# Optimization experiments

Measured on AMD Instinct MI355X. Metric: run time of the kernel, lower is better.

The kernel has to match this reference:

```python
import jax, jax.numpy as jnp
import numpy as np

N_NODES = 50000
N_REL = 4
N_EDGES = 400000
IN_F, HID_F, OUT_F = 128, 128, 64


def _graphconv(h, s, d, W, b, n_nodes):
    """DGL GraphConv, norm='both': D_dst^{-1/2} A D_src^{-1/2} h W + b.
    Degrees clamped to min 1 (DGL behavior for isolated nodes)."""
    ones = jnp.ones(s.shape[0], h.dtype)
    deg_out = jnp.clip(jax.ops.segment_sum(ones, s, num_segments=n_nodes), 1.0)
    deg_in = jnp.clip(jax.ops.segment_sum(ones, d, num_segments=n_nodes), 1.0)
    # scale src features, transform first (weight applied pre-aggregation)
    hw = (h * jax.lax.rsqrt(deg_out)[:, None]) @ W          # [N, out]
    msg = hw[s]                                              # gather  [E, out]
    agg = jax.ops.segment_sum(msg, d, num_segments=n_nodes)  # scatter [N, out]
    return agg * jax.lax.rsqrt(deg_in)[:, None] + b


def _hetero_layer(h, src, dst, W, b):
    # HeteroGraphConv with aggregate='sum': sum per-relation GraphConv outputs
    n_nodes = h.shape[0]
    out = _graphconv(h, src[0], dst[0], W[0], b[0], n_nodes)
    for r in range(1, W.shape[0]):
        out = out + _graphconv(h, src[r], dst[r], W[r], b[r], n_nodes)
    return out


def setup_inputs() -> dict:
    key = jax.random.key(0)
    k = jax.random.split(key, 6)
    x = jax.random.normal(k[0], (N_NODES, IN_F), dtype=jnp.float32)
    src = jax.random.randint(k[1], (N_REL, N_EDGES), 0, N_NODES, dtype=jnp.int32)
    dst = jax.random.randint(k[2], (N_REL, N_EDGES), 0, N_NODES, dtype=jnp.int32)
    W1 = jax.random.normal(k[3], (N_REL, IN_F, HID_F), dtype=jnp.float32) / np.sqrt(IN_F)
    b1 = jnp.zeros((N_REL, HID_F), dtype=jnp.float32)
    W2 = jax.random.normal(k[4], (N_REL, HID_F, OUT_F), dtype=jnp.float32) / np.sqrt(HID_F)
    b2 = jnp.zeros((N_REL, OUT_F), dtype=jnp.float32)
    return {"x": x, "src": src, "dst": dst, "W1": W1, "b1": b1, "W2": W2, "b2": b2}


def reference(x, src, dst, W1, b1, W2, b2):
    h = _hetero_layer(x, src, dst, W1, b1)
    h = jax.nn.relu(h)
    return _hetero_layer(h, src, dst, W2, b2)
```

## Files before the change

### kernel.cpp

```cpp
#include <hip/hip_runtime.h>
#include <hip/hip_bf16.h>

#define N_NODES 50000
#define N_REL 4
#define N_EDGES 400000
#define CHUNK 1024
#define NCHUNK ((N_NODES + CHUNK - 1) / CHUNK)

#define EB 32
#define ECH (N_EDGES / EB)
#define NR 8
#define RNG (N_NODES / NR)

using short8 = __attribute__((ext_vector_type(8))) short;
using f32x4 = __attribute__((ext_vector_type(4))) float;

static __device__ inline unsigned short f2bf(float f) {
  unsigned u = __float_as_uint(f);
  unsigned r = (u + 0x7FFFu + ((u >> 16) & 1u)) >> 16;
  return (unsigned short)r;
}
static __device__ inline float bf2f(unsigned short b) {
  return __uint_as_float(((unsigned)b) << 16);
}
static __device__ inline void fma_bf2(unsigned w, float ds, float& a0,
                                      float& a1) {
  float lo = __uint_as_float(w << 16);
  float hi = __uint_as_float(w & 0xffff0000u);
  a0 = fmaf(lo, ds, a0);
  a1 = fmaf(hi, ds, a1);
}

__global__ __launch_bounds__(256) void k_hist(const int* __restrict__ src,
                                              const int* __restrict__ dst,
                                              unsigned short* __restrict__ Hs,
                                              unsigned short* __restrict__ Hd) {
  const int range = blockIdx.x % NR;
  const int chunk = (blockIdx.x / NR) % EB;
  const int rel = blockIdx.x / (NR * EB);
  __shared__ unsigned int ldsS[RNG / 2], ldsD[RNG / 2];
  for (int i = threadIdx.x; i < RNG / 2; i += 256) {
    ldsS[i] = 0u;
    ldsD[i] = 0u;
  }
  __syncthreads();
  const int n0 = range * RNG;
  const int* sp = src + (size_t)rel * N_EDGES + chunk * ECH;
  const int* dp = dst + (size_t)rel * N_EDGES + chunk * ECH;
  for (int e = threadIdx.x; e < ECH; e += 256) {
    int s = sp[e] - n0;
    if ((unsigned)s < RNG) atomicAdd(&ldsS[s >> 1], 1u << ((s & 1) * 16));
    int d = dp[e] - n0;
    if ((unsigned)d < RNG) atomicAdd(&ldsD[d >> 1], 1u << ((d & 1) * 16));
  }
  __syncthreads();
  unsigned int* HsO =
      (unsigned int*)(Hs + ((size_t)rel * EB + chunk) * N_NODES + n0);
  unsigned int* HdO =
      (unsigned int*)(Hd + ((size_t)rel * EB + chunk) * N_NODES + n0);
  for (int i = threadIdx.x; i < RNG / 2; i += 256) {
    HsO[i] = ldsS[i];
    HdO[i] = ldsD[i];
  }
}

__global__ __launch_bounds__(256) void k_reduce_m(
    const unsigned short* __restrict__ Hs, unsigned short* __restrict__ Hd,
    int* __restrict__ cnt_m, float* __restrict__ dso,
    float* __restrict__ dsi) {
  int n = blockIdx.x * 256 + threadIdx.x;
  if (n >= N_NODES) return;
#pragma unroll
  for (int r = 0; r < N_REL; ++r) {
    int so = 0;
#pragma unroll
    for (int b = 0; b < EB; ++b) so += Hs[((size_t)r * EB + b) * N_NODES + n];
    dso[r * N_NODES + n] = rsqrtf((float)(so < 1 ? 1 : so));
  }
  int run = 0;
#pragma unroll
  for (int r = 0; r < N_REL; ++r) {
    int start = run;
#pragma unroll
    for (int b = 0; b < EB; ++b) {
      size_t off = ((size_t)r * EB + b) * N_NODES + n;
      int v = Hd[off];
      Hd[off] = (unsigned short)run;
      run += v;
    }
    int di = run - start;
    dsi[r * N_NODES + n] = rsqrtf((float)(di < 1 ? 1 : di));
  }
  cnt_m[n] = run;
}

__global__ __launch_bounds__(256) void k_chunk_sums(
    const int* __restrict__ cnt_m, int* __restrict__ chunkSums) {
  int c = blockIdx.x;
  int t = threadIdx.x;
  int base = c * CHUNK + t * 4;
  int s = 0;
#pragma unroll
  for (int j = 0; j < 4; ++j) {
    int n = base + j;
    if (n < N_NODES) s += cnt_m[n];
  }
  __shared__ int lds[256];
  lds[t] = s;
  __syncthreads();
  for (int off = 128; off > 0; off >>= 1) {
    if (t < off) lds[t] += lds[t + off];
    __syncthreads();
  }
  if (t == 0) chunkSums[c] = lds[0];
}

__global__ __launch_bounds__(64) void k_scan_chunks(int* __restrict__ chunkSums,
                                                    int* __restrict__ row_ptr) {
  if (threadIdx.x == 0) {
    int running = 0;
    for (int c = 0; c < NCHUNK; ++c) {
      int v = chunkSums[c];
      chunkSums[c] = running;
      running += v;
    }
    row_ptr[N_NODES] = N_REL * N_EDGES;
  }
}

__global__ __launch_bounds__(256) void k_scan_within(
    const int* __restrict__ cnt_m, const int* __restrict__ chunkOff,
    int* __restrict__ row_ptr) {
  int c = blockIdx.x;
  int t = threadIdx.x;
  int base = c * CHUNK + t * 4;
  int v[4];
#pragma unroll
  for (int j = 0; j < 4; ++j) {
    int n = base + j;
    v[j] = (n < N_NODES) ? cnt_m[n] : 0;
  }
  int total = v[0] + v[1] + v[2] + v[3];
  __shared__ int lds[256];
  lds[t] = total;
  __syncthreads();
  for (int off = 1; off < 256; off <<= 1) {
    int add = (t >= off) ? lds[t - off] : 0;
    __syncthreads();
    lds[t] += add;
    __syncthreads();
  }
  int thrExcl = lds[t] - total + chunkOff[c];
  int pre = 0;
#pragma unroll
  for (int j = 0; j < 4; ++j) {
    int n = base + j;
    if (n < N_NODES) row_ptr[n] = thrExcl + pre;
    pre += v[j];
  }
}

__global__ __launch_bounds__(256) void k_fill2m(
    const int* __restrict__ src, const int* __restrict__ dst,
    const unsigned short* __restrict__ Hd, const int* __restrict__ row_ptr,
    int* __restrict__ sorted) {
  const int range = blockIdx.x % NR;
  const int chunk = (blockIdx.x / NR) % EB;
  const int rel = blockIdx.x / (NR * EB);
  __shared__ unsigned int cur[RNG];
  const int n0 = range * RNG;
  const int* rp = row_ptr + n0;
  const unsigned short* pref = Hd + ((size_t)rel * EB + chunk) * N_NODES + n0;
  for (int i = threadIdx.x; i < RNG; i += 256)
    cur[i] = (unsigned)(rp[i] + pref[i]);
  __syncthreads();
  const int* sp = src + (size_t)rel * N_EDGES + chunk * ECH;
  const int* dp = dst + (size_t)rel * N_EDGES + chunk * ECH;
  for (int e = threadIdx.x; e < ECH; e += 256) {
    int d = dp[e] - n0;
    if ((unsigned)d < RNG) {
      unsigned pos = atomicAdd(&cur[d], 1u);
      sorted[pos] = (sp[e] << 2) | rel;
    }
  }
}

__global__ __launch_bounds__(256) void k_prep_x(const float* __restrict__ x,
                                                unsigned short* __restrict__ xb) {
  int i = blockIdx.x * 256 + threadIdx.x;
  if (i >= N_NODES * 16) return;
  const float4* p = (const float4*)x + (size_t)i * 2;
  float4 v0 = p[0], v1 = p[1];
  unsigned short pk[8] = {f2bf(v0.x), f2bf(v0.y), f2bf(v0.z), f2bf(v0.w),
                          f2bf(v1.x), f2bf(v1.y), f2bf(v1.z), f2bf(v1.w)};
  *(uint4*)(xb + (size_t)i * 8) = *(uint4*)pk;
}

__global__ __launch_bounds__(128) void k_prep_w(const float* __restrict__ W1,
                                                const float* __restrict__ W2,
                                                unsigned short* __restrict__ Wt1,
                                                unsigned short* __restrict__ Wt2) {
  int b = blockIdx.x;
  int k = threadIdx.x;
  if (b < 512) {
    int p = b >> 8, c = b & 255;
    int r = p * 2 + (c >> 7), cc = c & 127;
    Wt1[(size_t)b * 128 + k] = f2bf(W1[(size_t)r * 16384 + k * 128 + cc]);
  } else {
    int c = b - 512;
    int r = c >> 6, cc = c & 63;
    Wt2[(size_t)c * 128 + k] = f2bf(W2[(size_t)r * 8192 + k * 64 + cc]);
  }
}

template <int REL_COLS>
__global__ __launch_bounds__(256, 2) void k_gemm_mfma(
    const unsigned short* __restrict__ A, const unsigned short* __restrict__ Wt,
    const float* __restrict__ dsoBase, unsigned short* __restrict__ C,
    int cstride, int M) {
  __shared__ unsigned short Alds[64 * 128];
  __shared__ unsigned short Wlds[256 * 128];
  const int tid = threadIdx.x;
  const int wid = tid >> 6, lane = tid & 63;
  const int rowBase = blockIdx.x * 64;
  const unsigned short* WtP = Wt + (size_t)blockIdx.y * 256 * 128;
  const float* dsoP = dsoBase + (size_t)blockIdx.y * 2 * N_NODES;
  unsigned short* CP = C + (size_t)blockIdx.y * 256;

#pragma unroll
  for (int i = 0; i < 4; ++i) {
    int cid = tid + i * 256;
    int row = cid >> 4, kg = cid & 15;
    int grow = rowBase + row;
    uint4 v = make_uint4(0, 0, 0, 0);
    if (grow < M) v = *(const uint4*)(A + (size_t)grow * 128 + kg * 8);
    *(uint4*)(Alds + row * 128 + ((kg ^ (row & 7)) * 8)) = v;
  }
#pragma unroll
  for (int i = 0; i < 16; ++i) {
    int cid = tid + i * 256;
    int row = cid >> 4, kg = cid & 15;
    uint4 v = *(const uint4*)(WtP + (size_t)row * 128 + kg * 8);
    *(uint4*)(Wlds + row * 128 + ((kg ^ (row & 7)) * 8)) = v;
  }
  __syncthreads();

  f32x4 acc[4][4];
#pragma unroll
  for (int i = 0; i < 4; ++i)
#pragma unroll
    for (int j = 0; j < 4; ++j) acc[i][j] = (f32x4){0.f, 0.f, 0.f, 0.f};

  const int lrow = lane & 15;
  const int khalf = lane >> 4;
#pragma unroll
  for (int k0 = 0; k0 < 4; ++k0) {
    int kg = k0 * 4 + khalf;
    short8 a[4], b[4];
#pragma unroll
    for (int i = 0; i < 4; ++i) {
      int row = i * 16 + lrow;
      a[i] = *(const short8*)(Alds + row * 128 + ((kg ^ (row & 7)) * 8));
    }
#pragma unroll
    for (int j = 0; j < 4; ++j) {
      int wrow = wid * 64 + j * 16 + lrow;
      b[j] = *(const short8*)(Wlds + wrow * 128 + ((kg ^ (wrow & 7)) * 8));
    }
#pragma unroll
    for (int i = 0; i < 4; ++i)
#pragma unroll
      for (int j = 0; j < 4; ++j)
        acc[i][j] = __builtin_amdgcn_mfma_f32_16x16x32_bf16(a[i], b[j],
                                                            acc[i][j], 0, 0, 0);
  }

#pragma unroll
  for (int i = 0; i < 4; ++i) {
#pragma unroll
    for (int j = 0; j < 4; ++j) {
      int col = wid * 64 + j * 16 + (lane & 15);
      const float* dsoCol = dsoP + (size_t)(col / REL_COLS) * N_NODES;
#pragma unroll
      for (int r = 0; r < 4; ++r) {
        int grow = rowBase + i * 16 + (lane >> 4) * 4 + r;
        if (grow < M)
          CP[(size_t)grow * cstride + col] = f2bf(acc[i][j][r] * dsoCol[grow]);
      }
    }
  }
}

static __device__ inline float dsel(int r, float d0, float d1, float d2,
                                    float d3) {
  float lo = (r & 1) ? d1 : d0;
  float hi = (r & 1) ? d3 : d2;
  return (r & 2) ? hi : lo;
}

__global__ __launch_bounds__(256) void k_gather1m(
    const unsigned short* __restrict__ Y, const int* __restrict__ row_ptr,
    const int* __restrict__ sortedm, const float* __restrict__ dsi,
    const float* __restrict__ b1, unsigned int* __restrict__ h1) {
  const int wave = threadIdx.x >> 6, lane = threadIdx.x & 63;
  const int g = lane & 31;
  const int node = blockIdx.x * 8 + wave * 2 + (lane >> 5);
  const int beg = row_ptr[node], end = row_ptr[node + 1];
  const float d0 = dsi[node], d1 = dsi[N_NODES + node];
  const float d2 = dsi[2 * N_NODES + node], d3 = dsi[3 * N_NODES + node];
  float a0[8] = {0, 0, 0, 0, 0, 0, 0, 0}, a1[8] = {0, 0, 0, 0, 0, 0, 0, 0};
  float a2[8] = {0, 0, 0, 0, 0, 0, 0, 0}, a3[8] = {0, 0, 0, 0, 0, 0, 0, 0};
  for (int base = beg; base < end; base += 32) {
    int n = end - base;
    if (n > 32) n = 32;
    int my = (g < n) ? sortedm[base + g] : 0;
    int j = 0;
    for (; j + 7 < n; j += 8) {
#pragma unroll
      for (int k = 0; k < 8; ++k) {
        int u = __shfl(my, j + k, 32);
        float ds = dsel(u & 3, d0, d1, d2, d3);
        uint2 w = *(const uint2*)(Y + (size_t)u * 128 + g * 4);
        fma_bf2(w.x, ds, a0[k], a1[k]);
        fma_bf2(w.y, ds, a2[k], a3[k]);
      }
    }
    for (; j < n; ++j) {
      int u = __shfl(my, j, 32);
      float ds = dsel(u & 3, d0, d1, d2, d3);
      uint2 w = *(const uint2*)(Y + (size_t)u * 128 + g * 4);
      fma_bf2(w.x, ds, a0[0], a1[0]);
      fma_bf2(w.y, ds, a2[0], a3[0]);
    }
  }
  float t0 = ((a0[0] + a0[1]) + (a0[2] + a0[3])) + ((a0[4] + a0[5]) + (a0[6] + a0[7]));
  float t1 = ((a1[0] + a1[1]) + (a1[2] + a1[3])) + ((a1[4] + a1[5]) + (a1[6] + a1[7]));
  float t2 = ((a2[0] + a2[1]) + (a2[2] + a2[3])) + ((a2[4] + a2[5]) + (a2[6] + a2[7]));
  float t3 = ((a3[0] + a3[1]) + (a3[2] + a3[3])) + ((a3[4] + a3[5]) + (a3[6] + a3[7]));
#pragma unroll
  for (int r = 0; r < 4; ++r) {
    float4 bb = *(const float4*)(b1 + r * 128 + g * 4);
    t0 += bb.x;
    t1 += bb.y;
    t2 += bb.z;
    t3 += bb.w;
  }
  uint2 pk;
  pk.x = (unsigned)f2bf(fmaxf(t0, 0.f)) | ((unsigned)f2bf(fmaxf(t1, 0.f)) << 16);
  pk.y = (unsigned)f2bf(fmaxf(t2, 0.f)) | ((unsigned)f2bf(fmaxf(t3, 0.f)) << 16);
  *((uint2*)h1 + (size_t)node * 32 + g) = pk;
}

__global__ __launch_bounds__(256) void k_gather2m(
    const unsigned short* __restrict__ Y, const int* __restrict__ row_ptr,
    const int* __restrict__ sortedm, const float* __restrict__ dsi,
    const float* __restrict__ b2, float* __restrict__ out) {
  const int wave = threadIdx.x >> 6, lane = threadIdx.x & 63;
  const int g = lane & 15;
  const int node = blockIdx.x * 16 + wave * 4 + (lane >> 4);
  const int beg = row_ptr[node], end = row_ptr[node + 1];
  const float d0 = dsi[node], d1 = dsi[N_NODES + node];
  const float d2 = dsi[2 * N_NODES + node], d3 = dsi[3 * N_NODES + node];
  float a0[8] = {0, 0, 0, 0, 0, 0, 0, 0}, a1[8] = {0, 0, 0, 0, 0, 0, 0, 0};
  float a2[8] = {0, 0, 0, 0, 0, 0, 0, 0}, a3[8] = {0, 0, 0, 0, 0, 0, 0, 0};
  for (int base = beg; base < end; base += 16) {
    int n = end - base;
    if (n > 16) n = 16;
    int my = (g < n) ? sortedm[base + g] : 0;
    int j = 0;
    for (; j + 7 < n; j += 8) {
#pragma unroll
      for (int k = 0; k < 8; ++k) {
        int u = __shfl(my, j + k, 16);
        float ds = dsel(u & 3, d0, d1, d2, d3);
        uint2 w = *(const uint2*)(Y + (size_t)u * 64 + g * 4);
        fma_bf2(w.x, ds, a0[k], a1[k]);
        fma_bf2(w.y, ds, a2[k], a3[k]);
      }
    }
    for (; j < n; ++j) {
      int u = __shfl(my, j, 16);
      float ds = dsel(u & 3, d0, d1, d2, d3);
      uint2 w = *(const uint2*)(Y + (size_t)u * 64 + g * 4);
      fma_bf2(w.x, ds, a0[0], a1[0]);
      fma_bf2(w.y, ds, a2[0], a3[0]);
    }
  }
  float t0 = ((a0[0] + a0[1]) + (a0[2] + a0[3])) + ((a0[4] + a0[5]) + (a0[6] + a0[7]));
  float t1 = ((a1[0] + a1[1]) + (a1[2] + a1[3])) + ((a1[4] + a1[5]) + (a1[6] + a1[7]));
  float t2 = ((a2[0] + a2[1]) + (a2[2] + a2[3])) + ((a2[4] + a2[5]) + (a2[6] + a2[7]));
  float t3 = ((a3[0] + a3[1]) + (a3[2] + a3[3])) + ((a3[4] + a3[5]) + (a3[6] + a3[7]));
#pragma unroll
  for (int r = 0; r < 4; ++r) {
    float4 bb = *(const float4*)(b2 + r * 64 + g * 4);
    t0 += bb.x;
    t1 += bb.y;
    t2 += bb.z;
    t3 += bb.w;
  }
  *(float4*)(out + (size_t)node * 64 + g * 4) = make_float4(t0, t1, t2, t3);
}

extern "C" void kernel_launch(void* const* d_in, const int* in_sizes, int n_in,
                              void* d_out, int out_size, void* d_ws,
                              size_t ws_size, hipStream_t stream) {
  const float* x  = (const float*)d_in[0];
  const int* src  = (const int*)d_in[1];
  const int* dst  = (const int*)d_in[2];
  const float* W1 = (const float*)d_in[3];
  const float* b1 = (const float*)d_in[4];
  const float* W2 = (const float*)d_in[5];
  const float* b2 = (const float*)d_in[6];
  float* out = (float*)d_out;

  char* wsb = (char*)d_ws;
  unsigned short* Hs = (unsigned short*)wsb;
  unsigned int* h1 = (unsigned int*)wsb;
  unsigned short* Hd = Hs + (size_t)N_REL * EB * N_NODES;
  unsigned short* xb = Hd + (size_t)N_REL * EB * N_NODES;
  unsigned short* Y = xb + (size_t)N_NODES * 128;
  char* tail = (char*)(Y + (size_t)N_NODES * 512);
  unsigned short* Wt1 = (unsigned short*)tail;
  unsigned short* Wt2 = Wt1 + 512 * 128;
  float* dso = (float*)(Wt2 + 256 * 128);
  float* dsi = dso + N_REL * N_NODES;
  int* cnt_m = (int*)(dsi + N_REL * N_NODES);
  int* row_ptr = cnt_m + N_NODES;
  int* chunkSums = row_ptr + (N_NODES + 1);
  int* sorted = chunkSums + 64;

  k_prep_x<<<(N_NODES * 16 + 255) / 256, 256, 0, stream>>>(x, xb);
  k_prep_w<<<768, 128, 0, stream>>>(W1, W2, Wt1, Wt2);
  k_hist<<<N_REL * EB * NR, 256, 0, stream>>>(src, dst, Hs, Hd);
  k_reduce_m<<<(N_NODES + 255) / 256, 256, 0, stream>>>(Hs, Hd, cnt_m, dso,
                                                        dsi);
  k_chunk_sums<<<NCHUNK, 256, 0, stream>>>(cnt_m, chunkSums);
  k_scan_chunks<<<1, 64, 0, stream>>>(chunkSums, row_ptr);
  k_scan_within<<<NCHUNK, 256, 0, stream>>>(cnt_m, chunkSums, row_ptr);
  k_fill2m<<<N_REL * EB * NR, 256, 0, stream>>>(src, dst, Hd, row_ptr, sorted);

  const int gemmGrid = (N_NODES + 63) / 64;
  k_gemm_mfma<128><<<dim3(gemmGrid, 2), 256, 0, stream>>>(xb, Wt1, dso, Y, 512,
                                                          N_NODES);
  k_gather1m<<<N_NODES / 8, 256, 0, stream>>>(Y, row_ptr, sorted, dsi, b1, h1);
  k_gemm_mfma<64><<<dim3(gemmGrid, 1), 256, 0, stream>>>(
      (unsigned short*)h1, Wt2, dso, Y, 256, N_NODES);
  k_gather2m<<<N_NODES / 16, 256, 0, stream>>>(Y, row_ptr, sorted, dsi, b2,
                                               out);
}
```

Before: 295.6 us.

## Aggregate raw features per relation before GEMM in layer one

Layer one now gathers bf16 input features per relation, scaling each by the source degree term, into a [N,512] buffer. A single K=512 GEMM then applies all four relation weights, adds the summed bias and applies ReLU. This replaces the old order of transforming first into a 512-wide Y and then gathering. Edge lists now store plain source ids, with per-node relation offsets (relOff) marking relation segments instead of rel tags packed into the low bits. The gathers stay the same width, but the agg buffer adds a write and a read, and the per-relation loops run shorter per-segment inner loops.

```diff
diff --git a/kernel.cpp b/kernel.cpp
--- a/kernel.cpp
+++ b/kernel.cpp
@@ -66,8 +66,8 @@
 
 __global__ __launch_bounds__(256) void k_reduce_m(
     const unsigned short* __restrict__ Hs, unsigned short* __restrict__ Hd,
-    int* __restrict__ cnt_m, float* __restrict__ dso,
-    float* __restrict__ dsi) {
+    int* __restrict__ cnt_m, float* __restrict__ dso, float* __restrict__ dsi,
+    ushort4* __restrict__ relOff) {
   int n = blockIdx.x * 256 + threadIdx.x;
   if (n >= N_NODES) return;
 #pragma unroll
@@ -78,9 +78,10 @@
     dso[r * N_NODES + n] = rsqrtf((float)(so < 1 ? 1 : so));
   }
   int run = 0;
+  unsigned short rs[4];
 #pragma unroll
   for (int r = 0; r < N_REL; ++r) {
-    int start = run;
+    rs[r] = (unsigned short)run;
 #pragma unroll
     for (int b = 0; b < EB; ++b) {
       size_t off = ((size_t)r * EB + b) * N_NODES + n;
@@ -88,10 +89,11 @@
       Hd[off] = (unsigned short)run;
       run += v;
     }
-    int di = run - start;
+    int di = run - rs[r];
     dsi[r * N_NODES + n] = rsqrtf((float)(di < 1 ? 1 : di));
   }
   cnt_m[n] = run;
+  relOff[n] = make_ushort4(rs[0], rs[1], rs[2], rs[3]);
 }
 
 __global__ __launch_bounds__(256) void k_chunk_sums(
@@ -180,7 +182,7 @@
     int d = dp[e] - n0;
     if ((unsigned)d < RNG) {
       unsigned pos = atomicAdd(&cur[d], 1u);
-      sorted[pos] = (sp[e] << 2) | rel;
+      sorted[pos] = sp[e];
     }
   }
 }
@@ -201,15 +203,145 @@
                                                 unsigned short* __restrict__ Wt1,
                                                 unsigned short* __restrict__ Wt2) {
   int b = blockIdx.x;
-  int k = threadIdx.x;
-  if (b < 512) {
-    int p = b >> 8, c = b & 255;
-    int r = p * 2 + (c >> 7), cc = c & 127;
-    Wt1[(size_t)b * 128 + k] = f2bf(W1[(size_t)r * 16384 + k * 128 + cc]);
+  int kk = threadIdx.x;
+  if (b < 128) {
+    int c = b;
+#pragma unroll
+    for (int r = 0; r < 4; ++r)
+      Wt1[(size_t)c * 512 + r * 128 + kk] =
+          f2bf(W1[(size_t)r * 16384 + kk * 128 + c]);
   } else {
-    int c = b - 512;
+    int c = b - 128;
     int r = c >> 6, cc = c & 63;
-    Wt2[(size_t)c * 128 + k] = f2bf(W2[(size_t)r * 8192 + k * 64 + cc]);
+    Wt2[(size_t)c * 128 + kk] = f2bf(W2[(size_t)r * 8192 + kk * 64 + cc]);
+  }
+}
+
+__global__ __launch_bounds__(256) void k_gather1a(
+    const unsigned short* __restrict__ xb, const int* __restrict__ row_ptr,
+    const ushort4* __restrict__ relOff, const int* __restrict__ sortedm,
+    const float* __restrict__ dso, const float* __restrict__ dsi,
+    unsigned int* __restrict__ agg) {
+  const int wave = threadIdx.x >> 6, lane = threadIdx.x & 63;
+  const int g = lane & 31;
+  const int node = blockIdx.x * 8 + wave * 2 + (lane >> 5);
+  const int rp = row_ptr[node], rp1 = row_ptr[node + 1];
+  const ushort4 ro = relOff[node];
+  const int beg[4] = {rp + ro.x, rp + ro.y, rp + ro.z, rp + ro.w};
+  const int end4[4] = {rp + ro.y, rp + ro.z, rp + ro.w, rp1};
+#pragma unroll
+  for (int r = 0; r < 4; ++r) {
+    const float* dsoR = dso + (size_t)r * N_NODES;
+    float a0[4] = {0, 0, 0, 0}, a1[4] = {0, 0, 0, 0};
+    float a2[4] = {0, 0, 0, 0}, a3[4] = {0, 0, 0, 0};
+    for (int base = beg[r]; base < end4[r]; base += 32) {
+      int n = end4[r] - base;
+      if (n > 32) n = 32;
+      int my = (g < n) ? sortedm[base + g] : 0;
+      int j = 0;
+      for (; j + 3 < n; j += 4) {
+#pragma unroll
+        for (int k = 0; k < 4; ++k) {
+          int s = __shfl(my, j + k, 32);
+          float ds = dsoR[s];
+          uint2 w = *(const uint2*)(xb + (size_t)s * 128 + g * 4);
+          fma_bf2(w.x, ds, a0[k], a1[k]);
+          fma_bf2(w.y, ds, a2[k], a3[k]);
+        }
+      }
+      for (; j < n; ++j) {
+        int s = __shfl(my, j, 32);
+        float ds = dsoR[s];
+        uint2 w = *(const uint2*)(xb + (size_t)s * 128 + g * 4);
+        fma_bf2(w.x, ds, a0[0], a1[0]);
+        fma_bf2(w.y, ds, a2[0], a3[0]);
+      }
+    }
+    float di = dsi[(size_t)r * N_NODES + node];
+    float t0 = ((a0[0] + a0[1]) + (a0[2] + a0[3])) * di;
+    float t1 = ((a1[0] + a1[1]) + (a1[2] + a1[3])) * di;
+    float t2 = ((a2[0] + a2[1]) + (a2[2] + a2[3])) * di;
+    float t3 = ((a3[0] + a3[1]) + (a3[2] + a3[3])) * di;
+    uint2 pk;
+    pk.x = (unsigned)f2bf(t0) | ((unsigned)f2bf(t1) << 16);
+    pk.y = (unsigned)f2bf(t2) | ((unsigned)f2bf(t3) << 16);
+    *((uint2*)agg + ((size_t)node * 4 + r) * 32 + g) = pk;
+  }
+}
+
+__global__ __launch_bounds__(256, 2) void k_gemm_h1(
+    const unsigned short* __restrict__ agg, const unsigned short* __restrict__ Wt,
+    const float* __restrict__ b1, unsigned short* __restrict__ h1, int M) {
+  __shared__ unsigned short Alds[64 * 128];
+  __shared__ unsigned short Wlds[128 * 128];
+  const int tid = threadIdx.x;
+  const int wid = tid >> 6, lane = tid & 63;
+  const int rowBase = blockIdx.x * 64;
+  const int lrow = lane & 15;
+  const int quarter = lane >> 4;
+
+  f32x4 acc[4][2];
+#pragma unroll
+  for (int i = 0; i < 4; ++i)
+#pragma unroll
+    for (int j = 0; j < 2; ++j) acc[i][j] = (f32x4){0.f, 0.f, 0.f, 0.f};
+
+  for (int k0 = 0; k0 < 4; ++k0) {
+    __syncthreads();
+#pragma unroll
+    for (int it = 0; it < 4; ++it) {
+      int cid = tid + it * 256;
+      int row = cid >> 4, kg = cid & 15;
+      int grow = rowBase + row;
+      uint4 v = make_uint4(0, 0, 0, 0);
+      if (grow < M)
+        v = *(const uint4*)(agg + (size_t)grow * 512 + k0 * 128 + kg * 8);
+      *(uint4*)(Alds + row * 128 + ((kg ^ (row & 7)) * 8)) = v;
+    }
+#pragma unroll
+    for (int it = 0; it < 8; ++it) {
+      int cid = tid + it * 256;
+      int c = cid >> 4, kg = cid & 15;
+      uint4 v = *(const uint4*)(Wt + (size_t)c * 512 + k0 * 128 + kg * 8);
+      *(uint4*)(Wlds + c * 128 + ((kg ^ (c & 7)) * 8)) = v;
+    }
+    __syncthreads();
+#pragma unroll
+    for (int kk = 0; kk < 4; ++kk) {
+      int kg = kk * 4 + quarter;
+      short8 a[4], b[2];
+#pragma unroll
+      for (int i = 0; i < 4; ++i) {
+        int row = i * 16 + lrow;
+        a[i] = *(const short8*)(Alds + row * 128 + ((kg ^ (row & 7)) * 8));
+      }
+#pragma unroll
+      for (int j = 0; j < 2; ++j) {
+        int c = wid * 32 + j * 16 + lrow;
+        b[j] = *(const short8*)(Wlds + c * 128 + ((kg ^ (c & 7)) * 8));
+      }
+#pragma unroll
+      for (int i = 0; i < 4; ++i)
+#pragma unroll
+        for (int j = 0; j < 2; ++j)
+          acc[i][j] = __builtin_amdgcn_mfma_f32_16x16x32_bf16(a[i], b[j],
+                                                              acc[i][j], 0, 0, 0);
+    }
+  }
+
+#pragma unroll
+  for (int j = 0; j < 2; ++j) {
+    int c = wid * 32 + j * 16 + lrow;
+    float bs = b1[c] + b1[128 + c] + b1[256 + c] + b1[384 + c];
+#pragma unroll
+    for (int i = 0; i < 4; ++i) {
+#pragma unroll
+      for (int r = 0; r < 4; ++r) {
+        int grow = rowBase + i * 16 + quarter * 4 + r;
+        if (grow < M)
+          h1[(size_t)grow * 128 + c] = f2bf(fmaxf(acc[i][j][r] + bs, 0.f));
+      }
+    }
   }
 }
 
@@ -223,9 +355,6 @@
   const int tid = threadIdx.x;
   const int wid = tid >> 6, lane = tid & 63;
   const int rowBase = blockIdx.x * 64;
-  const unsigned short* WtP = Wt + (size_t)blockIdx.y * 256 * 128;
-  const float* dsoP = dsoBase + (size_t)blockIdx.y * 2 * N_NODES;
-  unsigned short* CP = C + (size_t)blockIdx.y * 256;
 
 #pragma unroll
   for (int i = 0; i < 4; ++i) {
@@ -240,7 +369,7 @@
   for (int i = 0; i < 16; ++i) {
     int cid = tid + i * 256;
     int row = cid >> 4, kg = cid & 15;
-    uint4 v = *(const uint4*)(WtP + (size_t)row * 128 + kg * 8);
+    uint4 v = *(const uint4*)(Wt + (size_t)row * 128 + kg * 8);
     *(uint4*)(Wlds + row * 128 + ((kg ^ (row & 7)) * 8)) = v;
   }
   __syncthreads();
@@ -280,116 +409,61 @@
 #pragma unroll
     for (int j = 0; j < 4; ++j) {
       int col = wid * 64 + j * 16 + (lane & 15);
-      const float* dsoCol = dsoP + (size_t)(col / REL_COLS) * N_NODES;
+      const float* dsoCol = dsoBase + (size_t)(col / REL_COLS) * N_NODES;
 #pragma unroll
       for (int r = 0; r < 4; ++r) {
         int grow = rowBase + i * 16 + (lane >> 4) * 4 + r;
         if (grow < M)
-          CP[(size_t)grow * cstride + col] = f2bf(acc[i][j][r] * dsoCol[grow]);
-      }
-    }
-  }
-}
-
-static __device__ inline float dsel(int r, float d0, float d1, float d2,
-                                    float d3) {
-  float lo = (r & 1) ? d1 : d0;
-  float hi = (r & 1) ? d3 : d2;
-  return (r & 2) ? hi : lo;
-}
-
-__global__ __launch_bounds__(256) void k_gather1m(
-    const unsigned short* __restrict__ Y, const int* __restrict__ row_ptr,
-    const int* __restrict__ sortedm, const float* __restrict__ dsi,
-    const float* __restrict__ b1, unsigned int* __restrict__ h1) {
-  const int wave = threadIdx.x >> 6, lane = threadIdx.x & 63;
-  const int g = lane & 31;
-  const int node = blockIdx.x * 8 + wave * 2 + (lane >> 5);
-  const int beg = row_ptr[node], end = row_ptr[node + 1];
-  const float d0 = dsi[node], d1 = dsi[N_NODES + node];
-  const float d2 = dsi[2 * N_NODES + node], d3 = dsi[3 * N_NODES + node];
-  float a0[8] = {0, 0, 0, 0, 0, 0, 0, 0}, a1[8] = {0, 0, 0, 0, 0, 0, 0, 0};
-  float a2[8] = {0, 0, 0, 0, 0, 0, 0, 0}, a3[8] = {0, 0, 0, 0, 0, 0, 0, 0};
-  for (int base = beg; base < end; base += 32) {
-    int n = end - base;
-    if (n > 32) n = 32;
-    int my = (g < n) ? sortedm[base + g] : 0;
-    int j = 0;
-    for (; j + 7 < n; j += 8) {
-#pragma unroll
-      for (int k = 0; k < 8; ++k) {
-        int u = __shfl(my, j + k, 32);
-        float ds = dsel(u & 3, d0, d1, d2, d3);
-        uint2 w = *(const uint2*)(Y + (size_t)u * 128 + g * 4);
-        fma_bf2(w.x, ds, a0[k], a1[k]);
-        fma_bf2(w.y, ds, a2[k], a3[k]);
-      }
-    }
-    for (; j < n; ++j) {
-      int u = __shfl(my, j, 32);
-      float ds = dsel(u & 3, d0, d1, d2, d3);
-      uint2 w = *(const uint2*)(Y + (size_t)u * 128 + g * 4);
-      fma_bf2(w.x, ds, a0[0], a1[0]);
-      fma_bf2(w.y, ds, a2[0], a3[0]);
-    }
-  }
-  float t0 = ((a0[0] + a0[1]) + (a0[2] + a0[3])) + ((a0[4] + a0[5]) + (a0[6] + a0[7]));
-  float t1 = ((a1[0] + a1[1]) + (a1[2] + a1[3])) + ((a1[4] + a1[5]) + (a1[6] + a1[7]));
-  float t2 = ((a2[0] + a2[1]) + (a2[2] + a2[3])) + ((a2[4] + a2[5]) + (a2[6] + a2[7]));
-  float t3 = ((a3[0] + a3[1]) + (a3[2] + a3[3])) + ((a3[4] + a3[5]) + (a3[6] + a3[7]));
-#pragma unroll
-  for (int r = 0; r < 4; ++r) {
-    float4 bb = *(const float4*)(b1 + r * 128 + g * 4);
-    t0 += bb.x;
-    t1 += bb.y;
-    t2 += bb.z;
-    t3 += bb.w;
-  }
-  uint2 pk;
-  pk.x = (unsigned)f2bf(fmaxf(t0, 0.f)) | ((unsigned)f2bf(fmaxf(t1, 0.f)) << 16);
-  pk.y = (unsigned)f2bf(fmaxf(t2, 0.f)) | ((unsigned)f2bf(fmaxf(t3, 0.f)) << 16);
-  *((uint2*)h1 + (size_t)node * 32 + g) = pk;
+          C[(size_t)grow * cstride + col] = f2bf(acc[i][j][r] * dsoCol[grow]);
+      }
+    }
+  }
 }
 
 __global__ __launch_bounds__(256) void k_gather2m(
     const unsigned short* __restrict__ Y, const int* __restrict__ row_ptr,
-    const int* __restrict__ sortedm, const float* __restrict__ dsi,
-    const float* __restrict__ b2, float* __restrict__ out) {
+    const ushort4* __restrict__ relOff, const int* __restrict__ sortedm,
+    const float* __restrict__ dsi, const float* __restrict__ b2,
+    float* __restrict__ out) {
   const int wave = threadIdx.x >> 6, lane = threadIdx.x & 63;
   const int g = lane & 15;
   const int node = blockIdx.x * 16 + wave * 4 + (lane >> 4);
-  const int beg = row_ptr[node], end = row_ptr[node + 1];
-  const float d0 = dsi[node], d1 = dsi[N_NODES + node];
-  const float d2 = dsi[2 * N_NODES + node], d3 = dsi[3 * N_NODES + node];
-  float a0[8] = {0, 0, 0, 0, 0, 0, 0, 0}, a1[8] = {0, 0, 0, 0, 0, 0, 0, 0};
-  float a2[8] = {0, 0, 0, 0, 0, 0, 0, 0}, a3[8] = {0, 0, 0, 0, 0, 0, 0, 0};
-  for (int base = beg; base < end; base += 16) {
-    int n = end - base;
-    if (n > 16) n = 16;
-    int my = (g < n) ? sortedm[base + g] : 0;
-    int j = 0;
-    for (; j + 7 < n; j += 8) {
-#pragma unroll
-      for (int k = 0; k < 8; ++k) {
-        int u = __shfl(my, j + k, 16);
-        float ds = dsel(u & 3, d0, d1, d2, d3);
-        uint2 w = *(const uint2*)(Y + (size_t)u * 64 + g * 4);
-        fma_bf2(w.x, ds, a0[k], a1[k]);
-        fma_bf2(w.y, ds, a2[k], a3[k]);
-      }
-    }
-    for (; j < n; ++j) {
-      int u = __shfl(my, j, 16);
-      float ds = dsel(u & 3, d0, d1, d2, d3);
-      uint2 w = *(const uint2*)(Y + (size_t)u * 64 + g * 4);
-      fma_bf2(w.x, ds, a0[0], a1[0]);
-      fma_bf2(w.y, ds, a2[0], a3[0]);
-    }
-  }
-  float t0 = ((a0[0] + a0[1]) + (a0[2] + a0[3])) + ((a0[4] + a0[5]) + (a0[6] + a0[7]));
-  float t1 = ((a1[0] + a1[1]) + (a1[2] + a1[3])) + ((a1[4] + a1[5]) + (a1[6] + a1[7]));
-  float t2 = ((a2[0] + a2[1]) + (a2[2] + a2[3])) + ((a2[4] + a2[5]) + (a2[6] + a2[7]));
-  float t3 = ((a3[0] + a3[1]) + (a3[2] + a3[3])) + ((a3[4] + a3[5]) + (a3[6] + a3[7]));
+  const int rp = row_ptr[node], rp1 = row_ptr[node + 1];
+  const ushort4 ro = relOff[node];
+  const int beg[4] = {rp + ro.x, rp + ro.y, rp + ro.z, rp + ro.w};
+  const int end4[4] = {rp + ro.y, rp + ro.z, rp + ro.w, rp1};
+  float t0 = 0.f, t1 = 0.f, t2 = 0.f, t3 = 0.f;
+#pragma unroll
+  for (int r = 0; r < 4; ++r) {
+    float a0[4] = {0, 0, 0, 0}, a1[4] = {0, 0, 0, 0};
+    float a2[4] = {0, 0, 0, 0}, a3[4] = {0, 0, 0, 0};
+    for (int base = beg[r]; base < end4[r]; base += 16) {
+      int n = end4[r] - base;
+      if (n > 16) n = 16;
+      int my = (g < n) ? sortedm[base + g] : 0;
+      int j = 0;
+      for (; j + 3 < n; j += 4) {
+#pragma unroll
+        for (int k = 0; k < 4; ++k) {
+          int s = __shfl(my, j + k, 16);
+          uint2 w = *(const uint2*)(Y + ((size_t)s * 4 + r) * 64 + g * 4);
+          fma_bf2(w.x, 1.f, a0[k], a1[k]);
+          fma_bf2(w.y, 1.f, a2[k], a3[k]);
+        }
+      }
+      for (; j < n; ++j) {
+        int s = __shfl(my, j, 16);
+        uint2 w = *(const uint2*)(Y + ((size_t)s * 4 + r) * 64 + g * 4);
+        fma_bf2(w.x, 1.f, a0[0], a1[0]);
+        fma_bf2(w.y, 1.f, a2[0], a3[0]);
+      }
+    }
+    float di = dsi[(size_t)r * N_NODES + node];
+    t0 = fmaf((a0[0] + a0[1]) + (a0[2] + a0[3]), di, t0);
+    t1 = fmaf((a1[0] + a1[1]) + (a1[2] + a1[3]), di, t1);
+    t2 = fmaf((a2[0] + a2[1]) + (a2[2] + a2[3]), di, t2);
+    t3 = fmaf((a3[0] + a3[1]) + (a3[2] + a3[3]), di, t3);
+  }
 #pragma unroll
   for (int r = 0; r < 4; ++r) {
     float4 bb = *(const float4*)(b2 + r * 64 + g * 4);
@@ -415,36 +489,38 @@
 
   char* wsb = (char*)d_ws;
   unsigned short* Hs = (unsigned short*)wsb;
-  unsigned int* h1 = (unsigned int*)wsb;
+  unsigned short* h1 = (unsigned short*)wsb;
   unsigned short* Hd = Hs + (size_t)N_REL * EB * N_NODES;
   unsigned short* xb = Hd + (size_t)N_REL * EB * N_NODES;
-  unsigned short* Y = xb + (size_t)N_NODES * 128;
-  char* tail = (char*)(Y + (size_t)N_NODES * 512);
+  unsigned short* agg = xb + (size_t)N_NODES * 128;
+  unsigned short* Y2 = agg;
+  char* tail = (char*)(agg + (size_t)N_NODES * 512);
   unsigned short* Wt1 = (unsigned short*)tail;
-  unsigned short* Wt2 = Wt1 + 512 * 128;
+  unsigned short* Wt2 = Wt1 + 128 * 512;
   float* dso = (float*)(Wt2 + 256 * 128);
   float* dsi = dso + N_REL * N_NODES;
-  int* cnt_m = (int*)(dsi + N_REL * N_NODES);
+  ushort4* relOff = (ushort4*)(dsi + N_REL * N_NODES);
+  int* cnt_m = (int*)(relOff + N_NODES);
   int* row_ptr = cnt_m + N_NODES;
   int* chunkSums = row_ptr + (N_NODES + 1);
   int* sorted = chunkSums + 64;
 
   k_prep_x<<<(N_NODES * 16 + 255) / 256, 256, 0, stream>>>(x, xb);
-  k_prep_w<<<768, 128, 0, stream>>>(W1, W2, Wt1, Wt2);
+  k_prep_w<<<384, 128, 0, stream>>>(W1, W2, Wt1, Wt2);
   k_hist<<<N_REL * EB * NR, 256, 0, stream>>>(src, dst, Hs, Hd);
   k_reduce_m<<<(N_NODES + 255) / 256, 256, 0, stream>>>(Hs, Hd, cnt_m, dso,
-                                                        dsi);
+                                                        dsi, relOff);
   k_chunk_sums<<<NCHUNK, 256, 0, stream>>>(cnt_m, chunkSums);
   k_scan_chunks<<<1, 64, 0, stream>>>(chunkSums, row_ptr);
   k_scan_within<<<NCHUNK, 256, 0, stream>>>(cnt_m, chunkSums, row_ptr);
   k_fill2m<<<N_REL * EB * NR, 256, 0, stream>>>(src, dst, Hd, row_ptr, sorted);
 
-  const int gemmGrid = (N_NODES + 63) / 64;
-  k_gemm_mfma<128><<<dim3(gemmGrid, 2), 256, 0, stream>>>(xb, Wt1, dso, Y, 512,
-                                                          N_NODES);
-  k_gather1m<<<N_NODES / 8, 256, 0, stream>>>(Y, row_ptr, sorted, dsi, b1, h1);
-  k_gemm_mfma<64><<<dim3(gemmGrid, 1), 256, 0, stream>>>(
-      (unsigned short*)h1, Wt2, dso, Y, 256, N_NODES);
-  k_gather2m<<<N_NODES / 16, 256, 0, stream>>>(Y, row_ptr, sorted, dsi, b2,
-                                               out);
-}
+  k_gather1a<<<N_NODES / 8, 256, 0, stream>>>(xb, row_ptr, relOff, sorted, dso,
+                                              dsi, (unsigned int*)agg);
+  k_gemm_h1<<<(N_NODES + 63) / 64, 256, 0, stream>>>(agg, Wt1, b1, h1,
+                                                     N_NODES);
+  k_gemm_mfma<64><<<(N_NODES + 63) / 64, 256, 0, stream>>>(h1, Wt2, dso, Y2,
+                                                           256, N_NODES);
+  k_gather2m<<<N_NODES / 16, 256, 0, stream>>>(Y2, row_ptr, relOff, sorted,
+                                               dsi, b2, out);
+}
```

Result: faster. 275.2 us (-6.9%).
